# Optimization experiments

Measured on AMD Instinct MI355X. Metric: run time of the kernel, lower is better.

Reference implementation:

```python
import jax, jax.numpy as jnp
import numpy as np

INPUT_SIZE = 768
HIDDEN_SIZE = 16384
K_SPARSE = 32


def setup_inputs() -> dict:
    key = jax.random.key(0)
    kx, kw = jax.random.split(key)
    x = jax.random.normal(kx, (4096, INPUT_SIZE), dtype=jnp.float32)
    # encoder weight [hidden, input] (orthogonal init approximated by scaled normal)
    W = jax.random.normal(kw, (HIDDEN_SIZE, INPUT_SIZE), dtype=jnp.float32) / np.sqrt(INPUT_SIZE)
    b = jnp.zeros((HIDDEN_SIZE,), dtype=jnp.float32)
    return {"x": x, "W": W, "b": b}


def reference(x, W, b):
    # encoder GEMM: [B, in] @ [in, hidden] -> [B, hidden]
    pre = x @ W.T + b
    # topk threshold mask: keep values >= k-th largest per row
    top_vals = jax.lax.top_k(pre, K_SPARSE)[0]          # [B, k]
    thresh = top_vals[:, -1:]                           # [B, 1]
    encoded = pre * (pre >= thresh)                     # bool mask broadcasts to float
    # decode with row-L2-normalized encoder weights: encoded @ W_norm -> [B, in]
    W_norm = W / jnp.linalg.norm(W, axis=1, keepdims=True)
    decoded = encoded @ W_norm
    return decoded, encoded
```

## Files before the change

kernel.cpp:

```cpp
#include <hip/hip_runtime.h>
#include <hip/hip_bf16.h>
#include <math.h>

#define INPUT 768
#define HIDDEN 16384
#define ROWS 4096
#define KSP 32

#define SCREEN   1.9375f
#define SCREEN_Q 32256u
#define DELTA_Q  256u
#define SLOT     24
#define LCAP     1024
#define ACAP     64
#define SCAP     96
#define NCHUNK   128

typedef unsigned short u16;
typedef unsigned int u32;
typedef __attribute__((ext_vector_type(8))) short bf16x8;
typedef __attribute__((ext_vector_type(4))) float f32x4;

__device__ __forceinline__ u16 f2b(float v) {
    __hip_bfloat16 hb = __float2bfloat16(v);
    u16 h; __builtin_memcpy(&h, &hb, 2);
    return h;
}
__device__ __forceinline__ float b2f(u16 v) {
    return __uint_as_float(((u32)v) << 16);
}

__global__ __launch_bounds__(256) void convx_kernel(const float* __restrict__ x,
                                                    u16* __restrict__ xhi) {
    int row = blockIdx.x * 4 + (threadIdx.x >> 6);
    int lane = threadIdx.x & 63;
    const float4* src = (const float4*)(x + (size_t)row * INPUT);
    #pragma unroll
    for (int i = 0; i < 3; ++i) {
        int c = lane + i * 64;
        float4 v = src[c];
        ushort4 hv = make_ushort4(f2b(v.x), f2b(v.y), f2b(v.z), f2b(v.w));
        *(ushort4*)(xhi + (size_t)row * INPUT + c * 4) = hv;
    }
}

__global__ __launch_bounds__(256) void convw_kernel(const float* __restrict__ W,
                                                    u16* __restrict__ whi,
                                                    float* __restrict__ inv_norm) {
    int row = blockIdx.x * 4 + (threadIdx.x >> 6);
    int lane = threadIdx.x & 63;
    const float4* src = (const float4*)(W + (size_t)row * INPUT);
    float s = 0.f;
    #pragma unroll
    for (int i = 0; i < 3; ++i) {
        int c = lane + i * 64;
        float4 v = src[c];
        s += v.x * v.x + v.y * v.y + v.z * v.z + v.w * v.w;
        ushort4 hv = make_ushort4(f2b(v.x), f2b(v.y), f2b(v.z), f2b(v.w));
        *(ushort4*)(whi + (size_t)row * INPUT + c * 4) = hv;
    }
    for (int off = 32; off > 0; off >>= 1) s += __shfl_down(s, off, 64);
    if (lane == 0) inv_norm[row] = 1.0f / sqrtf(s);
}

#define TM 128
#define TN 128
#define BKK 64

#define GLDS(gp, lp)                                                  \
    __builtin_amdgcn_global_load_lds(                                 \
        (const __attribute__((address_space(1))) void*)(gp),          \
        (__attribute__((address_space(3))) void*)(lp), 16, 0, 0)

template <bool SCREENOUT>
__global__ __launch_bounds__(256) void gemm_mfma_kernel(const u16* __restrict__ xhi,
                                                        const u16* __restrict__ whi,
                                                        const float* __restrict__ bias,
                                                        float* __restrict__ preF,
                                                        float* __restrict__ enc,
                                                        u32* __restrict__ cntG,
                                                        u32* __restrict__ candG) {
    __shared__ u16 Ah[8192];
    __shared__ u16 Bh[8192];
    __shared__ u32 lcnt[TM];
    __shared__ u32 lslot[TM * SLOT];

    const int tid = threadIdx.x;
    const int lane = tid & 63;
    const int wave = tid >> 6;
    const int m0 = blockIdx.x * TM;
    const int n0 = blockIdx.y * TN;
    const int wm = wave >> 1;
    const int wn = wave & 1;

    if (SCREENOUT && tid < TM) lcnt[tid] = 0;

    f32x4 acc[4][4] = {};

    const int r0 = tid >> 2;
    const int cslot = tid & 3;
    const int swz0 = (r0 & 3) ^ ((r0 >> 2) & 3);
    const int k0 = (cslot ^ swz0) * 8;
    const size_t aOff0 = (size_t)(m0 + r0) * INPUT + k0;
    const size_t aOff1 = (size_t)(m0 + 64 + r0) * INPUT + k0;
    const size_t bOff0 = (size_t)(n0 + r0) * INPUT + k0;
    const size_t bOff1 = (size_t)(n0 + 64 + r0) * INPUT + k0;
    const int ldsW = wave * 512;

    const int fcol = lane & 15;
    const int quad = lane >> 4;
    const int swzf = (fcol & 3) ^ ((fcol >> 2) & 3);
    const int koff = (quad ^ swzf) * 8;

    for (int kt = 0; kt < INPUT; kt += BKK) {
        if (kt) __syncthreads();
        GLDS(xhi + aOff0 + kt,      Ah + ldsW);
        GLDS(xhi + aOff1 + kt,      Ah + 2048 + ldsW);
        GLDS(xhi + aOff0 + kt + 32, Ah + 4096 + ldsW);
        GLDS(xhi + aOff1 + kt + 32, Ah + 6144 + ldsW);
        GLDS(whi + bOff0 + kt,      Bh + ldsW);
        GLDS(whi + bOff1 + kt,      Bh + 2048 + ldsW);
        GLDS(whi + bOff0 + kt + 32, Bh + 4096 + ldsW);
        GLDS(whi + bOff1 + kt + 32, Bh + 6144 + ldsW);
        __syncthreads();

        #pragma unroll
        for (int h = 0; h < 2; ++h) {
            bf16x8 ah[4], bh[4];
            #pragma unroll
            for (int t = 0; t < 4; ++t) {
                int ai = h * 4096 + (wm * 64 + t * 16 + fcol) * 32 + koff;
                int bi = h * 4096 + (wn * 64 + t * 16 + fcol) * 32 + koff;
                ah[t] = *(const bf16x8*)(Ah + ai);
                bh[t] = *(const bf16x8*)(Bh + bi);
            }
            #pragma unroll
            for (int mt = 0; mt < 4; ++mt)
                #pragma unroll
                for (int nt = 0; nt < 4; ++nt)
                    acc[mt][nt] = __builtin_amdgcn_mfma_f32_16x16x32_bf16(ah[mt], bh[nt], acc[mt][nt], 0, 0, 0);
        }
    }

    float bv[4];
    #pragma unroll
    for (int nt = 0; nt < 4; ++nt) bv[nt] = bias[n0 + wn * 64 + nt * 16 + fcol];

    if (SCREENOUT) {
        float4 z4 = make_float4(0.f, 0.f, 0.f, 0.f);
        int c4 = tid & 31;
        int r8 = tid >> 5;
        #pragma unroll
        for (int i = 0; i < 16; ++i)
            *(float4*)(enc + (size_t)(m0 + r8 + i * 8) * HIDDEN + n0 + c4 * 4) = z4;

        #pragma unroll
        for (int mt = 0; mt < 4; ++mt) {
            int lrBase = wm * 64 + mt * 16 + quad * 4;
            #pragma unroll
            for (int nt = 0; nt < 4; ++nt) {
                int gn = n0 + wn * 64 + nt * 16 + fcol;
                #pragma unroll
                for (int rr = 0; rr < 4; ++rr) {
                    float v = acc[mt][nt][rr] + bv[nt];
                    if (v >= SCREEN) {
                        int lr = lrBase + rr;
                        float qf = fminf((v + 2.0f) * 8192.0f + 0.5f, 65535.0f);
                        u32 q = (u32)qf;
                        u32 pos = atomicAdd(&lcnt[lr], 1u);
                        if (pos < SLOT) lslot[lr * SLOT + pos] = (q << 16) | (u32)gn;
                    }
                }
            }
        }
        __syncthreads();

        const int nc = blockIdx.y;
        if (tid < TM) cntG[(size_t)nc * ROWS + m0 + tid] = min(lcnt[tid], (u32)SLOT);
        u32* dst = candG + (size_t)nc * ROWS * SLOT + (size_t)m0 * SLOT;
        for (int idx = tid; idx < TM * SLOT; idx += 256) dst[idx] = lslot[idx];
    } else {
        #pragma unroll
        for (int mt = 0; mt < 4; ++mt) {
            int gm = m0 + wm * 64 + mt * 16 + quad * 4;
            #pragma unroll
            for (int nt = 0; nt < 4; ++nt) {
                int gn = n0 + wn * 64 + nt * 16 + fcol;
                float* p = preF + (size_t)gm * HIDDEN + gn;
                #pragma unroll
                for (int r = 0; r < 4; ++r) p[(size_t)r * HIDDEN] = acc[mt][nt][r] + bv[nt];
            }
        }
    }
}

__global__ __launch_bounds__(256) void select_q_kernel(const u32* __restrict__ cntG,
                                                       const u32* __restrict__ candG,
                                                       float* __restrict__ enc,
                                                       const float* __restrict__ x,
                                                       const float* __restrict__ W,
                                                       const u16* __restrict__ whi,
                                                       const float* __restrict__ b,
                                                       const float* __restrict__ inv_norm,
                                                       float* __restrict__ dec) {
    __shared__ float xs[INPUT];
    __shared__ u32  scnt[NCHUNK];
    __shared__ u32  soff[NCHUNK];
    __shared__ u32  cl[LCAP];
    __shared__ int   aidx[ACAP];
    __shared__ float aex[ACAP];
    __shared__ int   scol[SCAP];
    __shared__ float sval[SCAP];
    __shared__ u32  wsum[4];
    __shared__ u32  ssum[4];
    __shared__ u32  s_n, s_amb, s_sel;
    __shared__ float red[4];

    const int tid = threadIdx.x;
    const int lane = tid & 63;
    const int wave = tid >> 6;
    const int r = blockIdx.x;

    if (tid == 0) { s_amb = 0; s_sel = 0; }
    #pragma unroll
    for (int i = 0; i < 3; ++i) xs[tid + i * 256] = x[(size_t)r * INPUT + tid + i * 256];
    if (tid < NCHUNK) scnt[tid] = cntG[(size_t)tid * ROWS + r];
    __syncthreads();

    if (tid == 0) {
        u32 t = 0;
        for (int c = 0; c < NCHUNK; ++c) { soff[c] = t; t += scnt[c]; }
        s_n = t;
    }
    __syncthreads();

    if (tid < NCHUNK) {
        int c = tid;
        u32 cnt_c = scnt[c];
        u32 off = soff[c];
        const u32* src = candG + (size_t)c * ROWS * SLOT + (size_t)r * SLOT;
        for (u32 s = 0; s < cnt_c; ++s) {
            u32 p = off + s;
            if (p < LCAP) cl[p] = src[s];
        }
    }
    __syncthreads();
    int n = (int)min(s_n, (u32)LCAP);

    u32 k[4];
    #pragma unroll
    for (int i = 0; i < 4; ++i) {
        int idx = tid + i * 256;
        k[i] = (idx < n) ? (cl[idx] >> 16) : 0u;
    }
    u32 lo = SCREEN_Q, hi = 65535u;
    for (int it = 0; it < 16; ++it) {
        u32 mid = (lo + hi + 1u) >> 1;
        int c = (k[0] >= mid) + (k[1] >= mid) + (k[2] >= mid) + (k[3] >= mid);
        for (int off = 32; off > 0; off >>= 1) c += __shfl_down(c, off, 64);
        if (lane == 0) wsum[wave] = (u32)c;
        __syncthreads();
        u32 total = wsum[0] + wsum[1] + wsum[2] + wsum[3];
        if (total >= (u32)KSP) lo = mid; else hi = mid - 1u;
        __syncthreads();
    }
    const u32 q32 = lo;
    const u32 hiQ = q32 + DELTA_Q;
    const u32 loQ = q32 - DELTA_Q;

    int sc = 0;
    #pragma unroll
    for (int i = 0; i < 4; ++i) {
        int idx = tid + i * 256;
        if (idx < n) {
            u32 q = cl[idx] >> 16;
            if (q > hiQ) ++sc;
            else if (q >= loQ) {
                u32 p = atomicAdd(&s_amb, 1u);
                if (p < ACAP) aidx[p] = (int)(cl[idx] & 0xFFFFu);
            }
        }
    }
    for (int off = 32; off > 0; off >>= 1) sc += __shfl_down(sc, off, 64);
    if (lane == 0) ssum[wave] = (u32)sc;
    __syncthreads();
    const int S = (int)(ssum[0] + ssum[1] + ssum[2] + ssum[3]);
    const int namb = (int)min(s_amb, (u32)ACAP);

    for (int c = wave; c < namb; c += 4) {
        int j = aidx[c];
        const float* wr = W + (size_t)j * INPUT;
        float s = 0.f;
        #pragma unroll
        for (int i = 0; i < 12; ++i) s += xs[lane + 64 * i] * wr[lane + 64 * i];
        for (int off = 32; off > 0; off >>= 1) s += __shfl_down(s, off, 64);
        if (lane == 0) aex[c] = s + b[j];
    }
    __syncthreads();

    const int kth = KSP - S;
    float myv = (tid < namb) ? aex[tid] : -1e30f;
    int rank = 0;
    for (int i = 0; i < namb; ++i) rank += (aex[i] > myv);
    float candv = (tid < namb && rank <= kth - 1) ? myv : 1e30f;
    for (int off = 32; off > 0; off >>= 1) candv = fminf(candv, __shfl_down(candv, off, 64));
    if (lane == 0) red[wave] = candv;
    __syncthreads();
    const float E = fminf(fminf(red[0], red[1]), fminf(red[2], red[3]));

    #pragma unroll
    for (int i = 0; i < 4; ++i) {
        int idx = tid + i * 256;
        if (idx < n) {
            u32 q = cl[idx] >> 16;
            if (q > hiQ) {
                u32 p = atomicAdd(&s_sel, 1u);
                if (p < SCAP) {
                    scol[p] = (int)(cl[idx] & 0xFFFFu);
                    sval[p] = (float)q * (1.0f / 8192.0f) - 2.0f;
                }
            }
        }
    }
    for (int c = tid; c < namb; c += 256) {
        if (aex[c] >= E) {
            u32 p = atomicAdd(&s_sel, 1u);
            if (p < SCAP) { scol[p] = aidx[c]; sval[p] = aex[c]; }
        }
    }
    __syncthreads();
    const int nsel = (int)min(s_sel, (u32)SCAP);

    float* erow = enc + (size_t)r * HIDDEN;
    for (int c = tid; c < nsel; c += 256) erow[scol[c]] = sval[c];

    float a0 = 0.f, a1 = 0.f, a2 = 0.f;
    for (int c = 0; c < nsel; ++c) {
        int j = scol[c];
        float sc_ = sval[c] * inv_norm[j];
        const u16* wr = whi + (size_t)j * INPUT;
        a0 += sc_ * b2f(wr[tid]);
        a1 += sc_ * b2f(wr[tid + 256]);
        a2 += sc_ * b2f(wr[tid + 512]);
    }
    float* drow = dec + (size_t)r * INPUT;
    drow[tid] = a0;
    drow[tid + 256] = a1;
    drow[tid + 512] = a2;
}

__global__ __launch_bounds__(256) void select_f_kernel(float* __restrict__ enc,
                                                       const float* __restrict__ x,
                                                       const float* __restrict__ W,
                                                       const float* __restrict__ b,
                                                       const float* __restrict__ inv_norm,
                                                       float* __restrict__ dec) {
    __shared__ float xs[INPUT];
    __shared__ uint2 cl[LCAP];
    __shared__ int   fidx[128];
    __shared__ float fex[128];
    __shared__ u32 wsum[4];
    __shared__ u32 s_n, s_f;
    __shared__ float red[4];

    const int tid = threadIdx.x;
    const int lane = tid & 63;
    const int wave = tid >> 6;
    const int r = blockIdx.x;
    float* erow = enc + (size_t)r * HIDDEN;

    if (tid == 0) { s_n = 0; s_f = 0; }
    #pragma unroll
    for (int i = 0; i < 3; ++i) xs[tid + i * 256] = x[(size_t)r * INPUT + tid + i * 256];
    __syncthreads();

    #pragma unroll
    for (int i = 0; i < 16; ++i) {
        float4 v = ((const float4*)erow)[tid + i * 256];
        int jbase = (tid + i * 256) * 4;
        float vv[4] = {v.x, v.y, v.z, v.w};
        #pragma unroll
        for (int c = 0; c < 4; ++c) {
            if (vv[c] >= SCREEN) {
                u32 p = atomicAdd(&s_n, 1u);
                if (p < LCAP) cl[p] = make_uint2((unsigned)(jbase + c), __float_as_uint(vv[c]));
            }
        }
    }
    __syncthreads();
    int n = (int)min(s_n, (u32)LCAP);

    float kv[4];
    #pragma unroll
    for (int i = 0; i < 4; ++i) {
        int idx = tid + i * 256;
        kv[i] = (idx < n) ? __uint_as_float(cl[idx].y) : 0.f;
    }
    float vlo = SCREEN, vhi = SCREEN + 16.0f;
    for (int it = 0; it < 16; ++it) {
        float mid = 0.5f * (vlo + vhi);
        int c = (kv[0] >= mid) + (kv[1] >= mid) + (kv[2] >= mid) + (kv[3] >= mid);
        for (int off = 32; off > 0; off >>= 1) c += __shfl_down(c, off, 64);
        if (lane == 0) wsum[wave] = (u32)c;
        __syncthreads();
        u32 total = wsum[0] + wsum[1] + wsum[2] + wsum[3];
        if (total >= (u32)KSP) vlo = mid; else vhi = mid;
        __syncthreads();
    }
    float tcand = vlo - 0.0625f;

    #pragma unroll
    for (int i = 0; i < 4; ++i) {
        int idx = tid + i * 256;
        if (idx < n && __uint_as_float(cl[idx].y) >= tcand) {
            u32 p = atomicAdd(&s_f, 1u);
            if (p < 128u) fidx[p] = (int)cl[idx].x;
        }
    }
    __syncthreads();
    int fn = (int)min(s_f, 128u);

    for (int c = wave; c < fn; c += 4) {
        int j = fidx[c];
        const float* wr = W + (size_t)j * INPUT;
        float s = 0.f;
        #pragma unroll
        for (int i = 0; i < 12; ++i) s += xs[lane + 64 * i] * wr[lane + 64 * i];
        for (int off = 32; off > 0; off >>= 1) s += __shfl_down(s, off, 64);
        if (lane == 0) fex[c] = s + b[j];
    }
    __syncthreads();

    float myv = (tid < fn) ? fex[tid] : -1e30f;
    int rank = 0;
    for (int i = 0; i < fn; ++i) rank += (fex[i] > myv);
    float candv = (tid < fn && rank <= 31) ? myv : 1e30f;
    for (int off = 32; off > 0; off >>= 1) candv = fminf(candv, __shfl_down(candv, off, 64));
    if (lane == 0) red[wave] = candv;
    __syncthreads();
    float thresh = fminf(fminf(red[0], red[1]), fminf(red[2], red[3]));

    float4 z4 = make_float4(0.f, 0.f, 0.f, 0.f);
    #pragma unroll
    for (int i = 0; i < 16; ++i) ((float4*)erow)[tid + i * 256] = z4;
    __syncthreads();
    for (int c = tid; c < fn; c += 256)
        if (fex[c] >= thresh) erow[fidx[c]] = fex[c];

    float a0 = 0.f, a1 = 0.f, a2 = 0.f;
    for (int c = 0; c < fn; ++c) {
        float v = fex[c];
        if (v >= thresh) {
            int j = fidx[c];
            float sc = v * inv_norm[j];
            const float* wr = W + (size_t)j * INPUT;
            a0 += sc * wr[tid];
            a1 += sc * wr[tid + 256];
            a2 += sc * wr[tid + 512];
        }
    }
    float* drow = dec + (size_t)r * INPUT;
    drow[tid] = a0;
    drow[tid + 256] = a1;
    drow[tid + 512] = a2;
}

#define BM 64
#define BN 64
#define BK 16

__global__ __launch_bounds__(256) void rownorm_kernel(const float* __restrict__ W,
                                                      float* __restrict__ inv_norm) {
    int row = blockIdx.x * 4 + (threadIdx.x >> 6);
    int lane = threadIdx.x & 63;
    const float* wr = W + (size_t)row * INPUT;
    float s = 0.f;
    for (int c = lane; c < INPUT; c += 64) { float v = wr[c]; s += v * v; }
    for (int off = 32; off > 0; off >>= 1) s += __shfl_down(s, off, 64);
    if (lane == 0) inv_norm[row] = 1.0f / sqrtf(s);
}

__global__ __launch_bounds__(256) void gemm1_kernel(const float* __restrict__ x,
                                                    const float* __restrict__ W,
                                                    const float* __restrict__ b,
                                                    float* __restrict__ pre) {
    __shared__ float As[BK][BM + 4];
    __shared__ float Bs[BK][BN + 4];
    int tid = threadIdx.x;
    int m0 = blockIdx.y * BM;
    int n0 = blockIdx.x * BN;
    int tx = tid & 15;
    int ty = tid >> 4;
    int lrow = tid >> 2;
    int lk4  = (tid & 3) * 4;

    const float* xa = x + (size_t)(m0 + lrow) * INPUT + lk4;
    const float* wb = W + (size_t)(n0 + lrow) * INPUT + lk4;

    float acc[4][4] = {};

    for (int kt = 0; kt < INPUT; kt += BK) {
        float4 av = *(const float4*)(xa + kt);
        float4 bv = *(const float4*)(wb + kt);
        As[lk4 + 0][lrow] = av.x; As[lk4 + 1][lrow] = av.y;
        As[lk4 + 2][lrow] = av.z; As[lk4 + 3][lrow] = av.w;
        Bs[lk4 + 0][lrow] = bv.x; Bs[lk4 + 1][lrow] = bv.y;
        Bs[lk4 + 2][lrow] = bv.z; Bs[lk4 + 3][lrow] = bv.w;
        __syncthreads();
        #pragma unroll
        for (int kk = 0; kk < BK; ++kk) {
            float4 a4 = *(const float4*)&As[kk][ty * 4];
            float4 b4 = *(const float4*)&Bs[kk][tx * 4];
            float a[4] = {a4.x, a4.y, a4.z, a4.w};
            float bb[4] = {b4.x, b4.y, b4.z, b4.w};
            #pragma unroll
            for (int i = 0; i < 4; ++i)
                #pragma unroll
                for (int j = 0; j < 4; ++j)
                    acc[i][j] += a[i] * bb[j];
        }
        __syncthreads();
    }

    float bvals[4];
    #pragma unroll
    for (int j = 0; j < 4; ++j) bvals[j] = b[n0 + tx * 4 + j];
    #pragma unroll
    for (int i = 0; i < 4; ++i) {
        int m = m0 + ty * 4 + i;
        float4 o;
        o.x = acc[i][0] + bvals[0];
        o.y = acc[i][1] + bvals[1];
        o.z = acc[i][2] + bvals[2];
        o.w = acc[i][3] + bvals[3];
        *(float4*)(pre + (size_t)m * HIDDEN + n0 + tx * 4) = o;
    }
}

extern "C" void kernel_launch(void* const* d_in, const int* in_sizes, int n_in,
                              void* d_out, int out_size, void* d_ws, size_t ws_size,
                              hipStream_t stream) {
    const float* x = (const float*)d_in[0];
    const float* W = (const float*)d_in[1];
    const float* b = (const float*)d_in[2];

    float* dec = (float*)d_out;
    float* enc = (float*)d_out + (size_t)ROWS * INPUT;

    float* inv_norm = (float*)d_ws;
    u16*   xhi      = (u16*)((char*)d_ws + 65536);
    u16*   whi      = xhi + (size_t)ROWS * INPUT;
    u32*   cntG     = (u32*)(whi + (size_t)HIDDEN * INPUT);
    u32*   candG    = cntG + (size_t)NCHUNK * ROWS;

    const size_t need_mid  = 65536 + (size_t)(ROWS + HIDDEN) * INPUT * 2;
    const size_t need_full = need_mid + (size_t)NCHUNK * ROWS * 4 * (1 + SLOT);

    if (ws_size >= need_full) {
        convx_kernel<<<ROWS / 4, 256, 0, stream>>>(x, xhi);
        convw_kernel<<<HIDDEN / 4, 256, 0, stream>>>(W, whi, inv_norm);
        gemm_mfma_kernel<true><<<dim3(ROWS / TM, HIDDEN / TN), 256, 0, stream>>>(
            xhi, whi, b, nullptr, enc, cntG, candG);
        select_q_kernel<<<ROWS, 256, 0, stream>>>(cntG, candG, enc, x, W, whi, b, inv_norm, dec);
    } else if (ws_size >= need_mid) {
        convx_kernel<<<ROWS / 4, 256, 0, stream>>>(x, xhi);
        convw_kernel<<<HIDDEN / 4, 256, 0, stream>>>(W, whi, inv_norm);
        gemm_mfma_kernel<false><<<dim3(ROWS / TM, HIDDEN / TN), 256, 0, stream>>>(
            xhi, whi, b, enc, nullptr, nullptr, nullptr);
        select_f_kernel<<<ROWS, 256, 0, stream>>>(enc, x, W, b, inv_norm, dec);
    } else {
        rownorm_kernel<<<HIDDEN / 4, 256, 0, stream>>>(W, inv_norm);
        gemm1_kernel<<<dim3(HIDDEN / BN, ROWS / BM), 256, 0, stream>>>(x, W, b, enc);
        select_f_kernel<<<ROWS, 256, 0, stream>>>(enc, x, W, b, inv_norm, dec);
    }
}
```

Baseline: 525.3 us.

## Fuse conversion kernels, split GEMM variants, parallelize select gather and decode

Merges the x and W bf16 conversion kernels into one launch, which removes a kernel boundary. The select kernel now gathers candidates with two threads per chunk. Its binary search double-buffers the warp sums so one barrier per iteration can be dropped. The decode is restructured so each wave handles a subset of the selected columns, reads packed bf16 pairs, and reduces through shared memory; this adds 12KB of LDS per block, which may lower occupancy.

```diff
diff --git a/kernel.cpp b/kernel.cpp
--- a/kernel.cpp
+++ b/kernel.cpp
@@ -30,37 +30,38 @@
     return __uint_as_float(((u32)v) << 16);
 }
 
-__global__ __launch_bounds__(256) void convx_kernel(const float* __restrict__ x,
-                                                    u16* __restrict__ xhi) {
-    int row = blockIdx.x * 4 + (threadIdx.x >> 6);
-    int lane = threadIdx.x & 63;
-    const float4* src = (const float4*)(x + (size_t)row * INPUT);
-    #pragma unroll
-    for (int i = 0; i < 3; ++i) {
-        int c = lane + i * 64;
-        float4 v = src[c];
-        ushort4 hv = make_ushort4(f2b(v.x), f2b(v.y), f2b(v.z), f2b(v.w));
-        *(ushort4*)(xhi + (size_t)row * INPUT + c * 4) = hv;
-    }
-}
-
-__global__ __launch_bounds__(256) void convw_kernel(const float* __restrict__ W,
-                                                    u16* __restrict__ whi,
-                                                    float* __restrict__ inv_norm) {
-    int row = blockIdx.x * 4 + (threadIdx.x >> 6);
-    int lane = threadIdx.x & 63;
-    const float4* src = (const float4*)(W + (size_t)row * INPUT);
-    float s = 0.f;
-    #pragma unroll
-    for (int i = 0; i < 3; ++i) {
-        int c = lane + i * 64;
-        float4 v = src[c];
-        s += v.x * v.x + v.y * v.y + v.z * v.z + v.w * v.w;
-        ushort4 hv = make_ushort4(f2b(v.x), f2b(v.y), f2b(v.z), f2b(v.w));
-        *(ushort4*)(whi + (size_t)row * INPUT + c * 4) = hv;
-    }
-    for (int off = 32; off > 0; off >>= 1) s += __shfl_down(s, off, 64);
-    if (lane == 0) inv_norm[row] = 1.0f / sqrtf(s);
+__global__ __launch_bounds__(256) void conv_kernel(const float* __restrict__ x,
+                                                   const float* __restrict__ W,
+                                                   u16* __restrict__ xhi,
+                                                   u16* __restrict__ whi,
+                                                   float* __restrict__ inv_norm) {
+    const int blk = blockIdx.x;
+    const int lane = threadIdx.x & 63;
+    if (blk < ROWS / 4) {
+        int row = blk * 4 + (threadIdx.x >> 6);
+        const float4* src = (const float4*)(x + (size_t)row * INPUT);
+        #pragma unroll
+        for (int i = 0; i < 3; ++i) {
+            int c = lane + i * 64;
+            float4 v = src[c];
+            ushort4 hv = make_ushort4(f2b(v.x), f2b(v.y), f2b(v.z), f2b(v.w));
+            *(ushort4*)(xhi + (size_t)row * INPUT + c * 4) = hv;
+        }
+    } else {
+        int row = (blk - ROWS / 4) * 4 + (threadIdx.x >> 6);
+        const float4* src = (const float4*)(W + (size_t)row * INPUT);
+        float s = 0.f;
+        #pragma unroll
+        for (int i = 0; i < 3; ++i) {
+            int c = lane + i * 64;
+            float4 v = src[c];
+            s += v.x * v.x + v.y * v.y + v.z * v.z + v.w * v.w;
+            ushort4 hv = make_ushort4(f2b(v.x), f2b(v.y), f2b(v.z), f2b(v.w));
+            *(ushort4*)(whi + (size_t)row * INPUT + c * 4) = hv;
+        }
+        for (int off = 32; off > 0; off >>= 1) s += __shfl_down(s, off, 64);
+        if (lane == 0) inv_norm[row] = 1.0f / sqrtf(s);
+    }
 }
 
 #define TM 128
@@ -72,14 +73,12 @@
         (const __attribute__((address_space(1))) void*)(gp),          \
         (__attribute__((address_space(3))) void*)(lp), 16, 0, 0)
 
-template <bool SCREENOUT>
-__global__ __launch_bounds__(256) void gemm_mfma_kernel(const u16* __restrict__ xhi,
-                                                        const u16* __restrict__ whi,
-                                                        const float* __restrict__ bias,
-                                                        float* __restrict__ preF,
-                                                        float* __restrict__ enc,
-                                                        u32* __restrict__ cntG,
-                                                        u32* __restrict__ candG) {
+__global__ __launch_bounds__(256) void gemm128_kernel(const u16* __restrict__ xhi,
+                                                      const u16* __restrict__ whi,
+                                                      const float* __restrict__ bias,
+                                                      float* __restrict__ enc,
+                                                      u32* __restrict__ cntG,
+                                                      u32* __restrict__ candG) {
     __shared__ u16 Ah[8192];
     __shared__ u16 Bh[8192];
     __shared__ u32 lcnt[TM];
@@ -93,7 +92,7 @@
     const int wm = wave >> 1;
     const int wn = wave & 1;
 
-    if (SCREENOUT && tid < TM) lcnt[tid] = 0;
+    if (tid < TM) lcnt[tid] = 0;
 
     f32x4 acc[4][4] = {};
 
@@ -146,52 +145,38 @@
     #pragma unroll
     for (int nt = 0; nt < 4; ++nt) bv[nt] = bias[n0 + wn * 64 + nt * 16 + fcol];
 
-    if (SCREENOUT) {
-        float4 z4 = make_float4(0.f, 0.f, 0.f, 0.f);
-        int c4 = tid & 31;
-        int r8 = tid >> 5;
-        #pragma unroll
-        for (int i = 0; i < 16; ++i)
-            *(float4*)(enc + (size_t)(m0 + r8 + i * 8) * HIDDEN + n0 + c4 * 4) = z4;
-
-        #pragma unroll
-        for (int mt = 0; mt < 4; ++mt) {
-            int lrBase = wm * 64 + mt * 16 + quad * 4;
+    float4 z4 = make_float4(0.f, 0.f, 0.f, 0.f);
+    int c4 = tid & 31;
+    int r8 = tid >> 5;
+    #pragma unroll
+    for (int i = 0; i < 16; ++i)
+        *(float4*)(enc + (size_t)(m0 + r8 + i * 8) * HIDDEN + n0 + c4 * 4) = z4;
+
+    #pragma unroll
+    for (int mt = 0; mt < 4; ++mt) {
+        int lrBase = wm * 64 + mt * 16 + quad * 4;
+        #pragma unroll
+        for (int nt = 0; nt < 4; ++nt) {
+            int gn = n0 + wn * 64 + nt * 16 + fcol;
             #pragma unroll
-            for (int nt = 0; nt < 4; ++nt) {
-                int gn = n0 + wn * 64 + nt * 16 + fcol;
-                #pragma unroll
-                for (int rr = 0; rr < 4; ++rr) {
-                    float v = acc[mt][nt][rr] + bv[nt];
-                    if (v >= SCREEN) {
-                        int lr = lrBase + rr;
-                        float qf = fminf((v + 2.0f) * 8192.0f + 0.5f, 65535.0f);
-                        u32 q = (u32)qf;
-                        u32 pos = atomicAdd(&lcnt[lr], 1u);
-                        if (pos < SLOT) lslot[lr * SLOT + pos] = (q << 16) | (u32)gn;
-                    }
+            for (int rr = 0; rr < 4; ++rr) {
+                float v = acc[mt][nt][rr] + bv[nt];
+                if (v >= SCREEN) {
+                    int lr = lrBase + rr;
+                    float qf = fminf((v + 2.0f) * 8192.0f + 0.5f, 65535.0f);
+                    u32 q = (u32)qf;
+                    u32 pos = atomicAdd(&lcnt[lr], 1u);
+                    if (pos < SLOT) lslot[lr * SLOT + pos] = (q << 16) | (u32)gn;
                 }
             }
         }
-        __syncthreads();
-
-        const int nc = blockIdx.y;
-        if (tid < TM) cntG[(size_t)nc * ROWS + m0 + tid] = min(lcnt[tid], (u32)SLOT);
-        u32* dst = candG + (size_t)nc * ROWS * SLOT + (size_t)m0 * SLOT;
-        for (int idx = tid; idx < TM * SLOT; idx += 256) dst[idx] = lslot[idx];
-    } else {
-        #pragma unroll
-        for (int mt = 0; mt < 4; ++mt) {
-            int gm = m0 + wm * 64 + mt * 16 + quad * 4;
-            #pragma unroll
-            for (int nt = 0; nt < 4; ++nt) {
-                int gn = n0 + wn * 64 + nt * 16 + fcol;
-                float* p = preF + (size_t)gm * HIDDEN + gn;
-                #pragma unroll
-                for (int r = 0; r < 4; ++r) p[(size_t)r * HIDDEN] = acc[mt][nt][r] + bv[nt];
-            }
-        }
-    }
+    }
+    __syncthreads();
+
+    const int nc = blockIdx.y;
+    if (tid < TM) cntG[(size_t)nc * ROWS + m0 + tid] = min(lcnt[tid], (u32)SLOT);
+    u32* dst = candG + (size_t)nc * ROWS * SLOT + (size_t)m0 * SLOT;
+    for (int idx = tid; idx < TM * SLOT; idx += 256) dst[idx] = lslot[idx];
 }
 
 __global__ __launch_bounds__(256) void select_q_kernel(const u32* __restrict__ cntG,
@@ -211,10 +196,11 @@
     __shared__ float aex[ACAP];
     __shared__ int   scol[SCAP];
     __shared__ float sval[SCAP];
-    __shared__ u32  wsum[4];
+    __shared__ u32  wsum[8];
     __shared__ u32  ssum[4];
     __shared__ u32  s_n, s_amb, s_sel;
     __shared__ float red[4];
+    __shared__ float dacc[4][INPUT];
 
     const int tid = threadIdx.x;
     const int lane = tid & 63;
@@ -234,14 +220,16 @@
     }
     __syncthreads();
 
-    if (tid < NCHUNK) {
-        int c = tid;
-        u32 cnt_c = scnt[c];
-        u32 off = soff[c];
-        const u32* src = candG + (size_t)c * ROWS * SLOT + (size_t)r * SLOT;
-        for (u32 s = 0; s < cnt_c; ++s) {
-            u32 p = off + s;
-            if (p < LCAP) cl[p] = src[s];
+    {
+        int c = tid >> 1;
+        if (c < NCHUNK) {
+            u32 cnt_c = scnt[c];
+            u32 off = soff[c];
+            const u32* src = candG + (size_t)c * ROWS * SLOT + (size_t)r * SLOT;
+            for (u32 s = (u32)(tid & 1); s < cnt_c; s += 2) {
+                u32 p = off + s;
+                if (p < LCAP) cl[p] = src[s];
+            }
         }
     }
     __syncthreads();
@@ -258,11 +246,11 @@
         u32 mid = (lo + hi + 1u) >> 1;
         int c = (k[0] >= mid) + (k[1] >= mid) + (k[2] >= mid) + (k[3] >= mid);
         for (int off = 32; off > 0; off >>= 1) c += __shfl_down(c, off, 64);
-        if (lane == 0) wsum[wave] = (u32)c;
+        u32* ws = wsum + (it & 1) * 4;
+        if (lane == 0) ws[wave] = (u32)c;
         __syncthreads();
-        u32 total = wsum[0] + wsum[1] + wsum[2] + wsum[3];
+        u32 total = ws[0] + ws[1] + ws[2] + ws[3];
         if (total >= (u32)KSP) lo = mid; else hi = mid - 1u;
-        __syncthreads();
     }
     const u32 q32 = lo;
     const u32 hiQ = q32 + DELTA_Q;
@@ -334,19 +322,109 @@
     float* erow = enc + (size_t)r * HIDDEN;
     for (int c = tid; c < nsel; c += 256) erow[scol[c]] = sval[c];
 
-    float a0 = 0.f, a1 = 0.f, a2 = 0.f;
-    for (int c = 0; c < nsel; ++c) {
+    float pe[6] = {0.f, 0.f, 0.f, 0.f, 0.f, 0.f};
+    float po[6] = {0.f, 0.f, 0.f, 0.f, 0.f, 0.f};
+    for (int c = wave; c < nsel; c += 4) {
         int j = scol[c];
         float sc_ = sval[c] * inv_norm[j];
-        const u16* wr = whi + (size_t)j * INPUT;
-        a0 += sc_ * b2f(wr[tid]);
-        a1 += sc_ * b2f(wr[tid + 256]);
-        a2 += sc_ * b2f(wr[tid + 512]);
-    }
+        const u32* wr = (const u32*)(whi + (size_t)j * INPUT);
+        #pragma unroll
+        for (int kk = 0; kk < 6; ++kk) {
+            u32 v = wr[lane + 64 * kk];
+            pe[kk] += sc_ * b2f((u16)(v & 0xFFFFu));
+            po[kk] += sc_ * b2f((u16)(v >> 16));
+        }
+    }
+    #pragma unroll
+    for (int kk = 0; kk < 6; ++kk) {
+        *(float2*)&dacc[wave][2 * (lane + 64 * kk)] = make_float2(pe[kk], po[kk]);
+    }
+    __syncthreads();
     float* drow = dec + (size_t)r * INPUT;
-    drow[tid] = a0;
-    drow[tid + 256] = a1;
-    drow[tid + 512] = a2;
+    #pragma unroll
+    for (int i = 0; i < 3; ++i) {
+        int col = tid + i * 256;
+        drow[col] = dacc[0][col] + dacc[1][col] + dacc[2][col] + dacc[3][col];
+    }
+}
+
+__global__ __launch_bounds__(256) void gemm_mfma_f32out_kernel(const u16* __restrict__ xhi,
+                                                               const u16* __restrict__ whi,
+                                                               const float* __restrict__ bias,
+                                                               float* __restrict__ preF) {
+    __shared__ u16 Ah[8192];
+    __shared__ u16 Bh[8192];
+
+    const int tid = threadIdx.x;
+    const int lane = tid & 63;
+    const int wave = tid >> 6;
+    const int m0 = blockIdx.x * TM;
+    const int n0 = blockIdx.y * TN;
+    const int wm = wave >> 1;
+    const int wn = wave & 1;
+
+    f32x4 acc[4][4] = {};
+
+    const int r0 = tid >> 2;
+    const int cslot = tid & 3;
+    const int swz0 = (r0 & 3) ^ ((r0 >> 2) & 3);
+    const int k0 = (cslot ^ swz0) * 8;
+    const size_t aOff0 = (size_t)(m0 + r0) * INPUT + k0;
+    const size_t aOff1 = (size_t)(m0 + 64 + r0) * INPUT + k0;
+    const size_t bOff0 = (size_t)(n0 + r0) * INPUT + k0;
+    const size_t bOff1 = (size_t)(n0 + 64 + r0) * INPUT + k0;
+    const int ldsW = wave * 512;
+
+    const int fcol = lane & 15;
+    const int quad = lane >> 4;
+    const int swzf = (fcol & 3) ^ ((fcol >> 2) & 3);
+    const int koff = (quad ^ swzf) * 8;
+
+    for (int kt = 0; kt < INPUT; kt += BKK) {
+        if (kt) __syncthreads();
+        GLDS(xhi + aOff0 + kt,      Ah + ldsW);
+        GLDS(xhi + aOff1 + kt,      Ah + 2048 + ldsW);
+        GLDS(xhi + aOff0 + kt + 32, Ah + 4096 + ldsW);
+        GLDS(xhi + aOff1 + kt + 32, Ah + 6144 + ldsW);
+        GLDS(whi + bOff0 + kt,      Bh + ldsW);
+        GLDS(whi + bOff1 + kt,      Bh + 2048 + ldsW);
+        GLDS(whi + bOff0 + kt + 32, Bh + 4096 + ldsW);
+        GLDS(whi + bOff1 + kt + 32, Bh + 6144 + ldsW);
+        __syncthreads();
+
+        #pragma unroll
+        for (int h = 0; h < 2; ++h) {
+            bf16x8 ah[4], bh[4];
+            #pragma unroll
+            for (int t = 0; t < 4; ++t) {
+                int ai = h * 4096 + (wm * 64 + t * 16 + fcol) * 32 + koff;
+                int bi = h * 4096 + (wn * 64 + t * 16 + fcol) * 32 + koff;
+                ah[t] = *(const bf16x8*)(Ah + ai);
+                bh[t] = *(const bf16x8*)(Bh + bi);
+            }
+            #pragma unroll
+            for (int mt = 0; mt < 4; ++mt)
+                #pragma unroll
+                for (int nt = 0; nt < 4; ++nt)
+                    acc[mt][nt] = __builtin_amdgcn_mfma_f32_16x16x32_bf16(ah[mt], bh[nt], acc[mt][nt], 0, 0, 0);
+        }
+    }
+
+    float bv[4];
+    #pragma unroll
+    for (int nt = 0; nt < 4; ++nt) bv[nt] = bias[n0 + wn * 64 + nt * 16 + fcol];
+
+    #pragma unroll
+    for (int mt = 0; mt < 4; ++mt) {
+        int gm = m0 + wm * 64 + mt * 16 + quad * 4;
+        #pragma unroll
+        for (int nt = 0; nt < 4; ++nt) {
+            int gn = n0 + wn * 64 + nt * 16 + fcol;
+            float* p = preF + (size_t)gm * HIDDEN + gn;
+            #pragma unroll
+            for (int r = 0; r < 4; ++r) p[(size_t)r * HIDDEN] = acc[mt][nt][r] + bv[nt];
+        }
+    }
 }
 
 __global__ __launch_bounds__(256) void select_f_kernel(float* __restrict__ enc,
@@ -557,16 +635,14 @@
     const size_t need_full = need_mid + (size_t)NCHUNK * ROWS * 4 * (1 + SLOT);
 
     if (ws_size >= need_full) {
-        convx_kernel<<<ROWS / 4, 256, 0, stream>>>(x, xhi);
-        convw_kernel<<<HIDDEN / 4, 256, 0, stream>>>(W, whi, inv_norm);
-        gemm_mfma_kernel<true><<<dim3(ROWS / TM, HIDDEN / TN), 256, 0, stream>>>(
-            xhi, whi, b, nullptr, enc, cntG, candG);
+        conv_kernel<<<(ROWS + HIDDEN) / 4, 256, 0, stream>>>(x, W, xhi, whi, inv_norm);
+        gemm128_kernel<<<dim3(ROWS / TM, HIDDEN / TN), 256, 0, stream>>>(
+            xhi, whi, b, enc, cntG, candG);
         select_q_kernel<<<ROWS, 256, 0, stream>>>(cntG, candG, enc, x, W, whi, b, inv_norm, dec);
     } else if (ws_size >= need_mid) {
-        convx_kernel<<<ROWS / 4, 256, 0, stream>>>(x, xhi);
-        convw_kernel<<<HIDDEN / 4, 256, 0, stream>>>(W, whi, inv_norm);
-        gemm_mfma_kernel<false><<<dim3(ROWS / TM, HIDDEN / TN), 256, 0, stream>>>(
-            xhi, whi, b, enc, nullptr, nullptr, nullptr);
+        conv_kernel<<<(ROWS + HIDDEN) / 4, 256, 0, stream>>>(x, W, xhi, whi, inv_norm);
+        gemm_mfma_f32out_kernel<<<dim3(ROWS / TM, HIDDEN / TN), 256, 0, stream>>>(
+            xhi, whi, b, enc);
         select_f_kernel<<<ROWS, 256, 0, stream>>>(enc, x, W, b, inv_norm, dec);
     } else {
         rownorm_kernel<<<HIDDEN / 4, 256, 0, stream>>>(W, inv_norm);
```

Result: slower. 538.1 us (+2.4%).
